# Performance work log

Hardware: AMD Instinct MI355X
Metric: run time of the kernel (lower is better)

The kernel has to match this reference:

```python
import jax, jax.numpy as jnp
import numpy as np

B, L, C = 128, 1000, 12      # batch, seq_len, input_channels
H = 128                       # lstm_hidden
DM, DS, DC = 128, 16, 4       # d_model, d_state, d_conv
DI = 2 * DM                   # d_inner = expand * d_model
DR = 8                        # dt_rank = ceil(d_model/16)
FC, NC = 128, 5               # fc_hidden_size, num_classes


def setup_inputs() -> dict:
    key = jax.random.key(0)
    ks = jax.random.split(key, 24)
    def rn(k, shape, fan):
        return jax.random.normal(k, shape, jnp.float32) / np.sqrt(fan)
    inp = {}
    inp["x"] = jax.random.normal(ks[0], (B, L, C), jnp.float32)
    # LSTM (single layer, batch_first) — PyTorch gate order i,f,g,o
    inp["W_ih"] = rn(ks[1], (4 * H, C), H)
    inp["W_hh"] = rn(ks[2], (4 * H, H), H)
    inp["b_ih"] = rn(ks[3], (4 * H,), H)
    inp["b_hh"] = rn(ks[4], (4 * H,), H)
    # input_proj: Linear(H, DM)
    inp["Wp"] = rn(ks[5], (DM, H), H)
    inp["bp"] = rn(ks[6], (DM,), H)
    # Mamba params
    inp["in_proj_w"] = rn(ks[7], (2 * DI, DM), DM)
    inp["conv_w"] = rn(ks[8], (DI, 1, DC), DC)        # depthwise conv kernel
    inp["conv_b"] = rn(ks[9], (DI,), DC)
    inp["x_proj_w"] = rn(ks[10], (DR + 2 * DS, DI), DI)
    inp["dt_proj_w"] = rn(ks[11], (DI, DR), DR)
    inp["dt_proj_b"] = rn(ks[12], (DI,), DR)
    inp["A_log"] = jnp.broadcast_to(jnp.log(jnp.arange(1, DS + 1, dtype=jnp.float32)), (DI, DS)).copy()
    inp["D"] = jnp.ones((DI,), jnp.float32)
    inp["out_proj_w"] = rn(ks[13], (DM, DI), DI)
    # classifier head
    inp["fc1_w"] = rn(ks[14], (FC, DM), DM)
    inp["fc1_b"] = rn(ks[15], (FC,), DM)
    inp["fc2_w"] = rn(ks[16], (NC, FC), FC)
    inp["fc2_b"] = rn(ks[17], (NC,), FC)
    return inp


def _lstm(x, W_ih, W_hh, b_ih, b_hh):
    b = b_ih + b_hh
    xg = jnp.einsum('blc,gc->blg', x, W_ih) + b  # precompute input gates (B,L,4H)
    def step(carry, xt):
        h, c = carry
        g = xt + h @ W_hh.T
        i, f, gg, o = jnp.split(g, 4, axis=-1)
        c = jax.nn.sigmoid(f) * c + jax.nn.sigmoid(i) * jnp.tanh(gg)
        h = jax.nn.sigmoid(o) * jnp.tanh(c)
        return (h, c), h
    h0 = jnp.zeros((x.shape[0], H), x.dtype)
    (_, _), hs = jax.lax.scan(step, (h0, h0), jnp.swapaxes(xg, 0, 1))
    return jnp.swapaxes(hs, 0, 1)  # (B,L,H)


def _mamba(u, in_proj_w, conv_w, conv_b, x_proj_w, dt_proj_w, dt_proj_b, A_log, D, out_proj_w):
    xz = jnp.einsum('bld,ed->ble', u, in_proj_w)           # (B,L,2*DI)
    xi, z = jnp.split(xz, 2, axis=-1)
    # causal depthwise conv1d over time
    xc = jnp.swapaxes(xi, 1, 2)                             # (B,DI,L)
    xc = jax.lax.conv_general_dilated(xc, conv_w, (1,), [(DC - 1, 0)],
                                      feature_group_count=DI,
                                      dimension_numbers=('NCH', 'OIH', 'NCH'))
    xc = xc + conv_b[None, :, None]
    xs = jax.nn.silu(jnp.swapaxes(xc, 1, 2))                # (B,L,DI)
    x_dbl = jnp.einsum('bld,ed->ble', xs, x_proj_w)         # (B,L,DR+2*DS)
    dt, Bm, Cm = jnp.split(x_dbl, [DR, DR + DS], axis=-1)
    delta = jax.nn.softplus(jnp.einsum('blr,dr->bld', dt, dt_proj_w) + dt_proj_b)  # (B,L,DI)
    A = -jnp.exp(A_log)                                     # (DI,DS)
    def step(h, inp):
        d_t, B_t, C_t, x_t = inp                            # (B,DI),(B,DS),(B,DS),(B,DI)
        dA = jnp.exp(d_t[:, :, None] * A)                   # (B,DI,DS)
        h = dA * h + (d_t * x_t)[:, :, None] * B_t[:, None, :]
        y = jnp.einsum('bds,bs->bd', h, C_t)
        return h, y
    h0 = jnp.zeros((u.shape[0], DI, DS), u.dtype)
    seq = (jnp.swapaxes(delta, 0, 1), jnp.swapaxes(Bm, 0, 1),
           jnp.swapaxes(Cm, 0, 1), jnp.swapaxes(xs, 0, 1))
    _, ys = jax.lax.scan(step, h0, seq)                     # (L,B,DI)
    y = jnp.swapaxes(ys, 0, 1) + xs * D
    y = y * jax.nn.silu(z)
    return jnp.einsum('bld,ed->ble', y, out_proj_w)         # (B,L,DM)


def reference(x, W_ih, W_hh, b_ih, b_hh, Wp, bp, in_proj_w, conv_w, conv_b,
              x_proj_w, dt_proj_w, dt_proj_b, A_log, D, out_proj_w,
              fc1_w, fc1_b, fc2_w, fc2_b):
    h = _lstm(x, W_ih, W_hh, b_ih, b_hh)
    m_in = jnp.einsum('blh,dh->bld', h, Wp) + bp
    m_out = _mamba(m_in, in_proj_w, conv_w, conv_b, x_proj_w,
                   dt_proj_w, dt_proj_b, A_log, D, out_proj_w)
    pooled = m_out.mean(axis=1)                             # (B,DM)
    hfc = jax.nn.relu(pooled @ fc1_w.T + fc1_b)             # dropout: eval mode (identity)
    return hfc @ fc2_w.T + fc2_b                            # (B,NC)
```

## Files before the change

kernel.cpp:

```cpp
#include <hip/hip_runtime.h>
#include <cstdint>
#include <cstddef>

constexpr int LSEQ = 1000;
constexpr int NB   = 128;
constexpr int CINP = 12;
constexpr int HID  = 128;
constexpr int NGATE = 4 * HID;
constexpr int DMOD = 128;
constexpr int DINN = 256;
constexpr int NCL  = 5;

typedef unsigned short ushort_t;
typedef _Float16 half2_t __attribute__((ext_vector_type(2)));

__device__ __forceinline__ float bf2f(ushort_t u) {
  uint32_t b = ((uint32_t)u) << 16;
  float f; __builtin_memcpy(&f, &b, 4); return f;
}
__device__ __forceinline__ ushort_t f2bf(float f) {
  uint32_t b; __builtin_memcpy(&b, &f, 4);
  uint32_t r = (b + 0x7fffu + ((b >> 16) & 1u)) >> 16;
  return (ushort_t)r;
}
__device__ __forceinline__ half2_t u2h2(uint32_t v) {
  half2_t h; __builtin_memcpy(&h, &v, 4); return h;
}
__device__ __forceinline__ uint32_t h22u(half2_t h) {
  uint32_t v; __builtin_memcpy(&v, &h, 4); return v;
}
__device__ __forceinline__ uint32_t bfpair_to_h2(uint32_t v) {
  half2_t h;
  h.x = (_Float16)bf2f((ushort_t)(v & 0xffff));
  h.y = (_Float16)bf2f((ushort_t)(v >> 16));
  return h22u(h);
}

#if __has_builtin(__builtin_amdgcn_fdot2)
__device__ __forceinline__ float FDOT2(half2_t a, half2_t b, float c) {
  return __builtin_amdgcn_fdot2(a, b, c, false);
}
#else
__device__ __forceinline__ float FDOT2(half2_t a, half2_t b, float c) {
  return c + (float)a.x * (float)b.x + (float)a.y * (float)b.y;
}
#endif

__device__ __forceinline__ void bar_lgkm() {
  asm volatile("s_waitcnt lgkmcnt(0)\n\ts_barrier" ::: "memory");
}

__global__ __launch_bounds__(256) void k0_weff(
    const float* __restrict__ ipw, const float* __restrict__ Wp,
    const float* __restrict__ bp, uint32_t* __restrict__ Weffh,
    float* __restrict__ beff) {
  int idx = blockIdx.x * 256 + threadIdx.x;
  if (idx < NGATE * 64) {
    int e = idx >> 6, j = idx & 63;
    float a0 = 0.f, a1 = 0.f;
    for (int d = 0; d < DMOD; ++d) {
      float w = ipw[e * DMOD + d];
      a0 += w * Wp[d * HID + 2 * j];
      a1 += w * Wp[d * HID + 2 * j + 1];
    }
    half2_t h; h.x = (_Float16)a0; h.y = (_Float16)a1;
    Weffh[idx] = h22u(h);
  }
  if (idx < NGATE) {
    float acc = 0.f;
    for (int d = 0; d < DMOD; ++d) acc += ipw[idx * DMOD + d] * bp[d];
    beff[idx] = acc;
  }
}

__global__ __launch_bounds__(256, 1) void k1_lstm(
    const float* __restrict__ x, const float* __restrict__ W_ih,
    const float* __restrict__ W_hh, const float* __restrict__ b_ih,
    const float* __restrict__ b_hh, ushort_t* __restrict__ hout) {
  __shared__ __align__(16) float x_sh[LSEQ * CINP];
  __shared__ __align__(16) ushort_t h_sh[HID];
  __shared__ float tg_sh[HID];
  __shared__ float so_sh[HID];
  const int t = threadIdx.x;
  const int u = t & 127;
  const int half = t >> 7;
  const int rA = u + half * 256;
  const int rB = rA + 128;
  const int b = blockIdx.x;

  const float4* xg4 = reinterpret_cast<const float4*>(x + (size_t)b * LSEQ * CINP);
  float4* xs4 = reinterpret_cast<float4*>(x_sh);
  for (int i = t; i < LSEQ * CINP / 4; i += 256) xs4[i] = xg4[i];

  half2_t wa2[64], wb2[64];
  {
    const float4* wa4 = reinterpret_cast<const float4*>(W_hh) + rA * (HID / 4);
    const float4* wb4 = reinterpret_cast<const float4*>(W_hh) + rB * (HID / 4);
#pragma unroll
    for (int k = 0; k < HID / 4; ++k) {
      float4 v = wa4[k];
      half2_t a; a.x = (_Float16)v.x; a.y = (_Float16)v.y;
      half2_t c; c.x = (_Float16)v.z; c.y = (_Float16)v.w;
      wa2[2 * k] = a; wa2[2 * k + 1] = c;
      float4 w = wb4[k];
      half2_t d; d.x = (_Float16)w.x; d.y = (_Float16)w.y;
      half2_t e; e.x = (_Float16)w.z; e.y = (_Float16)w.w;
      wb2[2 * k] = d; wb2[2 * k + 1] = e;
    }
  }
  float wia[CINP], wib[CINP];
#pragma unroll
  for (int c = 0; c < CINP; ++c) {
    wia[c] = W_ih[rA * CINP + c];
    wib[c] = W_ih[rB * CINP + c];
  }
  const float biasA = b_ih[rA] + b_hh[rA];
  const float biasB = b_ih[rB] + b_hh[rB];

  float cstate = 0.f;
  if (t < HID) h_sh[t] = 0;
  __syncthreads();

  for (int l = 0; l < LSEQ; ++l) {
    const float* xr = &x_sh[l * CINP];
    float pa0 = biasA, pa1 = 0.f, pa2 = 0.f, pa3 = 0.f;
    float pb0 = biasB, pb1 = 0.f, pb2 = 0.f, pb3 = 0.f;
#pragma unroll
    for (int c = 0; c < CINP; c += 4) {
      float x0 = xr[c], x1 = xr[c + 1], x2 = xr[c + 2], x3 = xr[c + 3];
      pa0 += x0 * wia[c];     pa1 += x1 * wia[c + 1];
      pa2 += x2 * wia[c + 2]; pa3 += x3 * wia[c + 3];
      pb0 += x0 * wib[c];     pb1 += x1 * wib[c + 1];
      pb2 += x2 * wib[c + 2]; pb3 += x3 * wib[c + 3];
    }
    const uint4* h4 = reinterpret_cast<const uint4*>(h_sh);
#pragma unroll
    for (int kk = 0; kk < 16; ++kk) {
      uint4 hv = h4[kk];
      half2_t h0 = u2h2(hv.x), h1 = u2h2(hv.y), h2 = u2h2(hv.z), h3 = u2h2(hv.w);
      pa0 = FDOT2(h0, wa2[4 * kk],     pa0);
      pa1 = FDOT2(h1, wa2[4 * kk + 1], pa1);
      pa2 = FDOT2(h2, wa2[4 * kk + 2], pa2);
      pa3 = FDOT2(h3, wa2[4 * kk + 3], pa3);
      pb0 = FDOT2(h0, wb2[4 * kk],     pb0);
      pb1 = FDOT2(h1, wb2[4 * kk + 1], pb1);
      pb2 = FDOT2(h2, wb2[4 * kk + 2], pb2);
      pb3 = FDOT2(h3, wb2[4 * kk + 3], pb3);
    }
    float gA = (pa0 + pa1) + (pa2 + pa3);
    float gB = (pb0 + pb1) + (pb2 + pb3);

    float si = 0.f, sf = 0.f;
    if (half) {
      float tg = 1.f - 2.f / (__expf(2.f * gA) + 1.f);
      float so = 1.f / (1.f + __expf(-gB));
      tg_sh[u] = tg;
      so_sh[u] = so;
    } else {
      si = 1.f / (1.f + __expf(-gA));
      sf = 1.f / (1.f + __expf(-gB));
    }
    bar_lgkm();
    if (!half) {
      cstate = sf * cstate + si * tg_sh[u];
      float th = 1.f - 2.f / (__expf(2.f * cstate) + 1.f);
      float hv = so_sh[u] * th;
      _Float16 hh = (_Float16)hv;
      ushort_t hb; __builtin_memcpy(&hb, &hh, 2);
      h_sh[u] = hb;
      hout[((size_t)b * LSEQ + l) * HID + u] = f2bf(hv);
    }
    bar_lgkm();
  }
}

__global__ __launch_bounds__(256) void k2f(
    const ushort_t* __restrict__ hbuf, const uint32_t* __restrict__ Weffh,
    const float* __restrict__ beff, const float* __restrict__ cw,
    const float* __restrict__ cb, ushort_t* __restrict__ xs,
    ushort_t* __restrict__ sz) {
  constexpr int S = 66;
  __shared__ __align__(16) uint32_t smem[2 * 64 * S];
  uint32_t* As = smem;
  uint32_t* Bs = smem + 64 * S;
  const int tid = threadIdx.x;
  const size_t m0 = (size_t)blockIdx.x * 64;
  const int n0 = blockIdx.y * 64;

  const uint4* h4g = reinterpret_cast<const uint4*>(hbuf);
  for (int i = tid; i < 64 * 16; i += 256) {
    int row = i >> 4, c = i & 15;
    uint4 v = h4g[(m0 + row) * 16 + c];
    uint32_t* p = &As[row * S + c * 4];
    p[0] = bfpair_to_h2(v.x); p[1] = bfpair_to_h2(v.y);
    p[2] = bfpair_to_h2(v.z); p[3] = bfpair_to_h2(v.w);
  }
  const uint4* w4g = reinterpret_cast<const uint4*>(Weffh);
  for (int i = tid; i < 64 * 16; i += 256) {
    int row = i >> 4, c = i & 15;
    uint4 v = w4g[(size_t)(n0 + row) * 16 + c];
    uint32_t* p = &Bs[row * S + c * 4];
    p[0] = v.x; p[1] = v.y; p[2] = v.z; p[3] = v.w;
  }
  __syncthreads();

  const int tx = tid & 15, ty = tid >> 4;
  float acc[4][4] = {};
  {
    const uint32_t* ap = &As[(ty * 4) * S];
    const uint32_t* bp = &Bs[(tx * 4) * S];
#pragma unroll 4
    for (int kk = 0; kk < 32; ++kk) {
      uint2 a0 = *reinterpret_cast<const uint2*>(&ap[kk * 2]);
      uint2 a1 = *reinterpret_cast<const uint2*>(&ap[S + kk * 2]);
      uint2 a2 = *reinterpret_cast<const uint2*>(&ap[2 * S + kk * 2]);
      uint2 a3 = *reinterpret_cast<const uint2*>(&ap[3 * S + kk * 2]);
      uint2 b0 = *reinterpret_cast<const uint2*>(&bp[kk * 2]);
      uint2 b1 = *reinterpret_cast<const uint2*>(&bp[S + kk * 2]);
      uint2 b2 = *reinterpret_cast<const uint2*>(&bp[2 * S + kk * 2]);
      uint2 b3 = *reinterpret_cast<const uint2*>(&bp[3 * S + kk * 2]);
      acc[0][0] = FDOT2(u2h2(a0.x), u2h2(b0.x), acc[0][0]);
      acc[0][1] = FDOT2(u2h2(a0.x), u2h2(b1.x), acc[0][1]);
      acc[0][2] = FDOT2(u2h2(a0.x), u2h2(b2.x), acc[0][2]);
      acc[0][3] = FDOT2(u2h2(a0.x), u2h2(b3.x), acc[0][3]);
      acc[1][0] = FDOT2(u2h2(a1.x), u2h2(b0.x), acc[1][0]);
      acc[1][1] = FDOT2(u2h2(a1.x), u2h2(b1.x), acc[1][1]);
      acc[1][2] = FDOT2(u2h2(a1.x), u2h2(b2.x), acc[1][2]);
      acc[1][3] = FDOT2(u2h2(a1.x), u2h2(b3.x), acc[1][3]);
      acc[2][0] = FDOT2(u2h2(a2.x), u2h2(b0.x), acc[2][0]);
      acc[2][1] = FDOT2(u2h2(a2.x), u2h2(b1.x), acc[2][1]);
      acc[2][2] = FDOT2(u2h2(a2.x), u2h2(b2.x), acc[2][2]);
      acc[2][3] = FDOT2(u2h2(a2.x), u2h2(b3.x), acc[2][3]);
      acc[3][0] = FDOT2(u2h2(a3.x), u2h2(b0.x), acc[3][0]);
      acc[3][1] = FDOT2(u2h2(a3.x), u2h2(b1.x), acc[3][1]);
      acc[3][2] = FDOT2(u2h2(a3.x), u2h2(b2.x), acc[3][2]);
      acc[3][3] = FDOT2(u2h2(a3.x), u2h2(b3.x), acc[3][3]);
      acc[0][0] = FDOT2(u2h2(a0.y), u2h2(b0.y), acc[0][0]);
      acc[0][1] = FDOT2(u2h2(a0.y), u2h2(b1.y), acc[0][1]);
      acc[0][2] = FDOT2(u2h2(a0.y), u2h2(b2.y), acc[0][2]);
      acc[0][3] = FDOT2(u2h2(a0.y), u2h2(b3.y), acc[0][3]);
      acc[1][0] = FDOT2(u2h2(a1.y), u2h2(b0.y), acc[1][0]);
      acc[1][1] = FDOT2(u2h2(a1.y), u2h2(b1.y), acc[1][1]);
      acc[1][2] = FDOT2(u2h2(a1.y), u2h2(b2.y), acc[1][2]);
      acc[1][3] = FDOT2(u2h2(a1.y), u2h2(b3.y), acc[1][3]);
      acc[2][0] = FDOT2(u2h2(a2.y), u2h2(b0.y), acc[2][0]);
      acc[2][1] = FDOT2(u2h2(a2.y), u2h2(b1.y), acc[2][1]);
      acc[2][2] = FDOT2(u2h2(a2.y), u2h2(b2.y), acc[2][2]);
      acc[2][3] = FDOT2(u2h2(a2.y), u2h2(b3.y), acc[2][3]);
      acc[3][0] = FDOT2(u2h2(a3.y), u2h2(b0.y), acc[3][0]);
      acc[3][1] = FDOT2(u2h2(a3.y), u2h2(b1.y), acc[3][1]);
      acc[3][2] = FDOT2(u2h2(a3.y), u2h2(b2.y), acc[3][2]);
      acc[3][3] = FDOT2(u2h2(a3.y), u2h2(b3.y), acc[3][3]);
    }
  }

  const int col = n0 + tx * 4;
  float4 be = *reinterpret_cast<const float4*>(&beff[col]);

  if (n0 >= 256) {
#pragma unroll
    for (int i = 0; i < 4; ++i) {
      size_t row = m0 + ty * 4 + i;
      float v0 = acc[i][0] + be.x, v1 = acc[i][1] + be.y;
      float v2 = acc[i][2] + be.z, v3 = acc[i][3] + be.w;
      ushort4 o;
      o.x = f2bf(v0 / (1.f + __expf(-v0)));
      o.y = f2bf(v1 / (1.f + __expf(-v1)));
      o.z = f2bf(v2 / (1.f + __expf(-v2)));
      o.w = f2bf(v3 / (1.f + __expf(-v3)));
      *reinterpret_cast<ushort4*>(&sz[row * 256 + (col - 256)]) = o;
    }
    return;
  }

  float haloval = 0.f;
  const int hc = tid & 63;
  if (tid < 192) {
    int hr = tid >> 6;
    long hrow = (long)m0 - 3 + hr;
    if (hrow < 0) hrow = 0;
    const uint4* hg = reinterpret_cast<const uint4*>(hbuf + (size_t)hrow * 128);
    const uint32_t* brow = &Bs[hc * S];
    float a0 = beff[n0 + hc], a1 = 0.f, a2 = 0.f, a3 = 0.f;
#pragma unroll
    for (int k = 0; k < 16; ++k) {
      uint4 hv = hg[k];
      a0 = FDOT2(u2h2(bfpair_to_h2(hv.x)), u2h2(brow[4 * k]),     a0);
      a1 = FDOT2(u2h2(bfpair_to_h2(hv.y)), u2h2(brow[4 * k + 1]), a1);
      a2 = FDOT2(u2h2(bfpair_to_h2(hv.z)), u2h2(brow[4 * k + 2]), a2);
      a3 = FDOT2(u2h2(bfpair_to_h2(hv.w)), u2h2(brow[4 * k + 3]), a3);
    }
    haloval = (a0 + a1) + (a2 + a3);
  }
  __syncthreads();

  float* X = reinterpret_cast<float*>(smem);
#pragma unroll
  for (int i = 0; i < 4; ++i) {
    int r = ty * 4 + i;
    float* q = &X[(r + 3) * 68 + tx * 4];
    q[0] = acc[i][0] + be.x; q[1] = acc[i][1] + be.y;
    q[2] = acc[i][2] + be.z; q[3] = acc[i][3] + be.w;
  }
  if (tid < 192) X[(tid >> 6) * 68 + hc] = haloval;
  __syncthreads();

  float cw0[4], cw1[4], cw2[4], cw3[4], cbv[4];
#pragma unroll
  for (int j = 0; j < 4; ++j) {
    int d = col + j;
    cw0[j] = cw[d * 4]; cw1[j] = cw[d * 4 + 1];
    cw2[j] = cw[d * 4 + 2]; cw3[j] = cw[d * 4 + 3];
    cbv[j] = cb[d];
  }
#pragma unroll
  for (int i = 0; i < 4; ++i) {
    int r = ty * 4 + i;
    size_t m = m0 + r;
    int l = (int)(m % LSEQ);
    const float* xr3 = &X[(r + 3) * 68 + tx * 4];
    ushort_t ov[4];
#pragma unroll
    for (int j = 0; j < 4; ++j) {
      float o0 = cbv[j];
      o0 += cw3[j] * xr3[j];
      if (l >= 1) o0 += cw2[j] * xr3[j - 68];
      if (l >= 2) o0 += cw1[j] * xr3[j - 136];
      if (l >= 3) o0 += cw0[j] * xr3[j - 204];
      ov[j] = f2bf(o0 / (1.f + __expf(-o0)));
    }
    ushort4 o; o.x = ov[0]; o.y = ov[1]; o.z = ov[2]; o.w = ov[3];
    *reinterpret_cast<ushort4*>(&xs[m * 256 + col]) = o;
  }
}

__global__ __launch_bounds__(256) void k4_xdbl(
    const ushort_t* __restrict__ xs, const float* __restrict__ xpw,
    float* __restrict__ dtg, float* __restrict__ bc) {
  constexpr int XSTR = 134;
  __shared__ __align__(16) uint32_t xsh[64 * XSTR];
  __shared__ __align__(16) uint32_t wsh[40 * 128];
  const int tid = threadIdx.x;
  const size_t r0 = (size_t)blockIdx.x * 64;

  for (int i = tid; i < 64 * 128; i += 256) {
    int row = i >> 7, kk = i & 127;
    uint32_t v = *reinterpret_cast<const uint32_t*>(&xs[(r0 + row) * 256 + kk * 2]);
    xsh[row * XSTR + kk] = bfpair_to_h2(v);
  }
  for (int i = tid; i < 40 * 128; i += 256) {
    int c = i >> 7, kk = i & 127;
    half2_t h;
    h.x = (_Float16)xpw[c * 256 + kk * 2];
    h.y = (_Float16)xpw[c * 256 + kk * 2 + 1];
    wsh[i] = h22u(h);
  }
  __syncthreads();

  const int row = tid & 63;
  const int cg = tid >> 6;
  float acc[10] = {};
  for (int kk2 = 0; kk2 < 64; ++kk2) {
    uint2 xv = *reinterpret_cast<const uint2*>(&xsh[row * XSTR + kk2 * 2]);
    half2_t x0 = u2h2(xv.x), x1 = u2h2(xv.y);
#pragma unroll
    for (int i = 0; i < 10; ++i) {
      uint2 wv = *reinterpret_cast<const uint2*>(&wsh[(cg + 4 * i) * 128 + kk2 * 2]);
      acc[i] = FDOT2(x0, u2h2(wv.x), acc[i]);
      acc[i] = FDOT2(x1, u2h2(wv.y), acc[i]);
    }
  }
#pragma unroll
  for (int i = 0; i < 10; ++i) {
    int c = cg + 4 * i;
    if (c < 8) dtg[(r0 + row) * 8 + c] = acc[i];
    else bc[(r0 + row) * 32 + (c - 8)] = acc[i];
  }
}

__global__ __launch_bounds__(256) void k5_scan(
    const float* __restrict__ dtg, const ushort_t* __restrict__ xs,
    const ushort_t* __restrict__ sz, const float* __restrict__ bc,
    const float* __restrict__ A_log, const float* __restrict__ Dv,
    const float* __restrict__ dtw, const float* __restrict__ dtb,
    float* __restrict__ ysum) {
  const int b  = blockIdx.x >> 3;
  const int d  = ((blockIdx.x & 7) << 5) + (threadIdx.x >> 3);
  const int sg = threadIdx.x & 7;

  const float Aa0 = -__expf(A_log[d * 16 + sg * 2]);
  const float Aa1 = -__expf(A_log[d * 16 + sg * 2 + 1]);
  float w8[8];
#pragma unroll
  for (int r = 0; r < 8; ++r) w8[r] = dtw[d * 8 + r];
  const float db = dtb[d];
  const float DD = Dv[d];

  float h0 = 0.f, h1 = 0.f;
  float acc = 0.f, accD = 0.f;
  const size_t base = (size_t)b * LSEQ;

  float4 dta_c = *reinterpret_cast<const float4*>(&dtg[base * 8]);
  float4 dtb_c = *reinterpret_cast<const float4*>(&dtg[base * 8 + 4]);
  float  xv_c  = bf2f(xs[base * 256 + d]);
  float  zv_c  = bf2f(sz[base * 256 + d]);
  float2 bv_c  = *reinterpret_cast<const float2*>(&bc[base * 32 + sg * 2]);
  float2 cv_c  = *reinterpret_cast<const float2*>(&bc[base * 32 + 16 + sg * 2]);

  for (int l = 0; l < LSEQ; ++l) {
    const size_t nrow = base + ((l + 1 < LSEQ) ? (l + 1) : l);
    float4 dta_n = *reinterpret_cast<const float4*>(&dtg[nrow * 8]);
    float4 dtb_n = *reinterpret_cast<const float4*>(&dtg[nrow * 8 + 4]);
    float  xv_n  = bf2f(xs[nrow * 256 + d]);
    float  zv_n  = bf2f(sz[nrow * 256 + d]);
    float2 bv_n  = *reinterpret_cast<const float2*>(&bc[nrow * 32 + sg * 2]);
    float2 cv_n  = *reinterpret_cast<const float2*>(&bc[nrow * 32 + 16 + sg * 2]);

    float a = db + dta_c.x * w8[0] + dta_c.y * w8[1] + dta_c.z * w8[2] + dta_c.w * w8[3]
                 + dtb_c.x * w8[4] + dtb_c.y * w8[5] + dtb_c.z * w8[6] + dtb_c.w * w8[7];
    float dl = (a > 20.f) ? a : __logf(1.f + __expf(a));
    float dx = dl * xv_c;
    h0 = __expf(dl * Aa0) * h0 + dx * bv_c.x;
    h1 = __expf(dl * Aa1) * h1 + dx * bv_c.y;
    acc += (h0 * cv_c.x + h1 * cv_c.y) * zv_c;
    accD += xv_c * zv_c;

    dta_c = dta_n; dtb_c = dtb_n;
    xv_c = xv_n; zv_c = zv_n; bv_c = bv_n; cv_c = cv_n;
  }
  if (sg == 0) acc += DD * accD;
  acc += __shfl_xor(acc, 1);
  acc += __shfl_xor(acc, 2);
  acc += __shfl_xor(acc, 4);
  if (sg == 0) ysum[b * 256 + d] = acc;
}

__global__ __launch_bounds__(128) void k6_head(
    const float* __restrict__ ysum, const float* __restrict__ opw,
    const float* __restrict__ fc1w, const float* __restrict__ fc1b,
    const float* __restrict__ fc2w, const float* __restrict__ fc2b,
    float* __restrict__ out) {
  __shared__ float ys[256], pool[128], fcs[128];
  const int b = blockIdx.x, t = threadIdx.x;
  for (int i = t; i < 256; i += 128) ys[i] = ysum[b * 256 + i];
  __syncthreads();
  float a = 0.f;
  for (int e = 0; e < 256; ++e) a += opw[t * 256 + e] * ys[e];
  pool[t] = a * (1.0f / (float)LSEQ);
  __syncthreads();
  float a1 = fc1b[t];
  for (int d2 = 0; d2 < 128; ++d2) a1 += fc1w[t * 128 + d2] * pool[d2];
  fcs[t] = fmaxf(a1, 0.f);
  __syncthreads();
  if (t < NCL) {
    float o = fc2b[t];
    for (int f = 0; f < 128; ++f) o += fc2w[t * 128 + f] * fcs[f];
    out[b * NCL + t] = o;
  }
}

extern "C" void kernel_launch(void* const* d_in, const int* in_sizes, int n_in,
                              void* d_out, int out_size, void* d_ws, size_t ws_size,
                              hipStream_t stream) {
  const float* x     = (const float*)d_in[0];
  const float* W_ih  = (const float*)d_in[1];
  const float* W_hh  = (const float*)d_in[2];
  const float* b_ih  = (const float*)d_in[3];
  const float* b_hh  = (const float*)d_in[4];
  const float* Wp    = (const float*)d_in[5];
  const float* bp    = (const float*)d_in[6];
  const float* ipw   = (const float*)d_in[7];
  const float* cw    = (const float*)d_in[8];
  const float* cb    = (const float*)d_in[9];
  const float* xpw   = (const float*)d_in[10];
  const float* dtw   = (const float*)d_in[11];
  const float* dtb   = (const float*)d_in[12];
  const float* A_log = (const float*)d_in[13];
  const float* Dv    = (const float*)d_in[14];
  const float* opw   = (const float*)d_in[15];
  const float* fc1w  = (const float*)d_in[16];
  const float* fc1b  = (const float*)d_in[17];
  const float* fc2w  = (const float*)d_in[18];
  const float* fc2b  = (const float*)d_in[19];
  float* out = (float*)d_out;

  const size_t A_WEFF = 131072;
  const size_t A_BEFF = 4096, A_YSUM = 131072;
  const size_t A_HBUF = (size_t)NB * LSEQ * HID * 2;
  const size_t A_XS   = (size_t)NB * LSEQ * DINN * 2;
  const size_t A_SZ   = A_XS;
  const size_t A_DT   = (size_t)NB * LSEQ * 8 * 4;
  const size_t A_BC   = (size_t)NB * LSEQ * 32 * 4;
  const size_t FIXED_WIDE = A_WEFF + A_BEFF + A_YSUM + A_HBUF + A_XS + A_SZ + A_DT + A_BC;

  if (FIXED_WIDE <= ws_size) {
    char* p = (char*)d_ws;
    uint32_t* Weffh = (uint32_t*)p; p += A_WEFF;
    float*    beff = (float*)p;    p += A_BEFF;
    float*    ysum = (float*)p;    p += A_YSUM;
    ushort_t* hbuf = (ushort_t*)p; p += A_HBUF;
    ushort_t* xsb  = (ushort_t*)p; p += A_XS;
    ushort_t* szb  = (ushort_t*)p; p += A_SZ;
    float*    dtg  = (float*)p;    p += A_DT;
    float*    bcb  = (float*)p;    p += A_BC;

    const int rows = NB * LSEQ;
    hipLaunchKernelGGL(k0_weff, dim3(128), dim3(256), 0, stream, ipw, Wp, bp, Weffh, beff);
    hipLaunchKernelGGL(k1_lstm, dim3(NB), dim3(256), 0, stream, x, W_ih, W_hh, b_ih, b_hh, hbuf);
    hipLaunchKernelGGL(k2f, dim3(rows / 64, 8), dim3(256), 0, stream,
                       hbuf, Weffh, beff, cw, cb, xsb, szb);
    hipLaunchKernelGGL(k4_xdbl, dim3(rows / 64), dim3(256), 0, stream,
                       xsb, xpw, dtg, bcb);
    hipLaunchKernelGGL(k5_scan, dim3(NB * 8), dim3(256), 0, stream,
                       dtg, xsb, szb, bcb, A_log, Dv, dtw, dtb, ysum);
    hipLaunchKernelGGL(k6_head, dim3(NB), dim3(128), 0, stream,
                       ysum, opw, fc1w, fc1b, fc2w, fc2b, out);
    return;
  }

  const size_t FIXED = A_WEFF + A_BEFF + A_YSUM + A_HBUF;
  const size_t PERB = (size_t)LSEQ * DINN * 2 * 2 + (size_t)LSEQ * 8 * 4 + (size_t)LSEQ * 32 * 4;
  int nb = 8;
  for (int c = 64; c >= 8; c >>= 1) {
    if (FIXED + (size_t)c * PERB <= ws_size) { nb = c; break; }
  }
  char* p = (char*)d_ws;
  uint32_t* Weffh = (uint32_t*)p; p += A_WEFF;
  float*    beff = (float*)p;    p += A_BEFF;
  float*    ysum = (float*)p;    p += A_YSUM;
  ushort_t* hbuf = (ushort_t*)p; p += A_HBUF;
  ushort_t* xsb  = (ushort_t*)p; p += (size_t)nb * LSEQ * DINN * 2;
  ushort_t* szb  = (ushort_t*)p; p += (size_t)nb * LSEQ * DINN * 2;
  float*    dtg  = (float*)p;    p += (size_t)nb * LSEQ * 8 * 4;
  float*    bcb  = (float*)p;

  hipLaunchKernelGGL(k0_weff, dim3(128), dim3(256), 0, stream, ipw, Wp, bp, Weffh, beff);
  hipLaunchKernelGGL(k1_lstm, dim3(NB), dim3(256), 0, stream, x, W_ih, W_hh, b_ih, b_hh, hbuf);
  for (int b0 = 0; b0 < NB; b0 += nb) {
    const int rows = nb * LSEQ;
    hipLaunchKernelGGL(k2f, dim3(rows / 64, 8), dim3(256), 0, stream,
                       hbuf + (size_t)b0 * LSEQ * HID, Weffh, beff, cw, cb, xsb, szb);
    hipLaunchKernelGGL(k4_xdbl, dim3(rows / 64), dim3(256), 0, stream, xsb, xpw, dtg, bcb);
    hipLaunchKernelGGL(k5_scan, dim3(nb * 8), dim3(256), 0, stream,
                       dtg, xsb, szb, bcb, A_log, Dv, dtw, dtb, ysum + (size_t)b0 * DINN);
  }
  hipLaunchKernelGGL(k6_head, dim3(NB), dim3(128), 0, stream,
                     ysum, opw, fc1w, fc1b, fc2w, fc2b, out);
}
```

Before: 1.507 ms.

## Process two batch sequences per LSTM block to reuse register-resident weights

After: 2.005 ms. +33.1%, slower.

```diff
diff --git a/kernel.cpp b/kernel.cpp
--- a/kernel.cpp
+++ b/kernel.cpp
@@ -77,20 +77,26 @@
     const float* __restrict__ x, const float* __restrict__ W_ih,
     const float* __restrict__ W_hh, const float* __restrict__ b_ih,
     const float* __restrict__ b_hh, ushort_t* __restrict__ hout) {
-  __shared__ __align__(16) float x_sh[LSEQ * CINP];
-  __shared__ __align__(16) ushort_t h_sh[HID];
-  __shared__ float tg_sh[HID];
-  __shared__ float so_sh[HID];
+  __shared__ __align__(16) uint32_t x_sh[2][LSEQ * 6];
+  __shared__ __align__(16) ushort_t h_sh[2][HID];
+  __shared__ float tg_sh[2][HID];
+  __shared__ float so_sh[2][HID];
   const int t = threadIdx.x;
   const int u = t & 127;
   const int half = t >> 7;
   const int rA = u + half * 256;
   const int rB = rA + 128;
-  const int b = blockIdx.x;
-
-  const float4* xg4 = reinterpret_cast<const float4*>(x + (size_t)b * LSEQ * CINP);
-  float4* xs4 = reinterpret_cast<float4*>(x_sh);
-  for (int i = t; i < LSEQ * CINP / 4; i += 256) xs4[i] = xg4[i];
+  const int b0 = blockIdx.x * 2;
+
+#pragma unroll
+  for (int q = 0; q < 2; ++q) {
+    const float2* xg2 = reinterpret_cast<const float2*>(x + (size_t)(b0 + q) * LSEQ * CINP);
+    for (int i = t; i < LSEQ * 6; i += 256) {
+      float2 v = xg2[i];
+      half2_t h; h.x = (_Float16)v.x; h.y = (_Float16)v.y;
+      x_sh[q][i] = h22u(h);
+    }
+  }
 
   half2_t wa2[64], wb2[64];
   {
@@ -108,67 +114,97 @@
       wb2[2 * k] = d; wb2[2 * k + 1] = e;
     }
   }
-  float wia[CINP], wib[CINP];
-#pragma unroll
-  for (int c = 0; c < CINP; ++c) {
-    wia[c] = W_ih[rA * CINP + c];
-    wib[c] = W_ih[rB * CINP + c];
+  half2_t wiaP[6], wibP[6];
+#pragma unroll
+  for (int c = 0; c < 6; ++c) {
+    wiaP[c].x = (_Float16)W_ih[rA * CINP + 2 * c];
+    wiaP[c].y = (_Float16)W_ih[rA * CINP + 2 * c + 1];
+    wibP[c].x = (_Float16)W_ih[rB * CINP + 2 * c];
+    wibP[c].y = (_Float16)W_ih[rB * CINP + 2 * c + 1];
   }
   const float biasA = b_ih[rA] + b_hh[rA];
   const float biasB = b_ih[rB] + b_hh[rB];
 
-  float cstate = 0.f;
-  if (t < HID) h_sh[t] = 0;
+  float cs0 = 0.f, cs1 = 0.f;
+  if (t < HID) { h_sh[0][t] = 0; h_sh[1][t] = 0; }
   __syncthreads();
 
   for (int l = 0; l < LSEQ; ++l) {
-    const float* xr = &x_sh[l * CINP];
-    float pa0 = biasA, pa1 = 0.f, pa2 = 0.f, pa3 = 0.f;
-    float pb0 = biasB, pb1 = 0.f, pb2 = 0.f, pb3 = 0.f;
-#pragma unroll
-    for (int c = 0; c < CINP; c += 4) {
-      float x0 = xr[c], x1 = xr[c + 1], x2 = xr[c + 2], x3 = xr[c + 3];
-      pa0 += x0 * wia[c];     pa1 += x1 * wia[c + 1];
-      pa2 += x2 * wia[c + 2]; pa3 += x3 * wia[c + 3];
-      pb0 += x0 * wib[c];     pb1 += x1 * wib[c + 1];
-      pb2 += x2 * wib[c + 2]; pb3 += x3 * wib[c + 3];
-    }
-    const uint4* h4 = reinterpret_cast<const uint4*>(h_sh);
+    float pa[2][4], pb[2][4];
+#pragma unroll
+    for (int q = 0; q < 2; ++q) {
+      pa[q][0] = biasA; pa[q][1] = 0.f; pa[q][2] = 0.f; pa[q][3] = 0.f;
+      pb[q][0] = biasB; pb[q][1] = 0.f; pb[q][2] = 0.f; pb[q][3] = 0.f;
+      const uint32_t* xr = &x_sh[q][l * 6];
+#pragma unroll
+      for (int c = 0; c < 6; c += 2) {
+        half2_t xv0 = u2h2(xr[c]), xv1 = u2h2(xr[c + 1]);
+        pa[q][0] = FDOT2(xv0, wiaP[c],     pa[q][0]);
+        pa[q][1] = FDOT2(xv1, wiaP[c + 1], pa[q][1]);
+        pb[q][0] = FDOT2(xv0, wibP[c],     pb[q][0]);
+        pb[q][1] = FDOT2(xv1, wibP[c + 1], pb[q][1]);
+      }
+    }
+    const uint4* h40 = reinterpret_cast<const uint4*>(h_sh[0]);
+    const uint4* h41 = reinterpret_cast<const uint4*>(h_sh[1]);
 #pragma unroll
     for (int kk = 0; kk < 16; ++kk) {
-      uint4 hv = h4[kk];
-      half2_t h0 = u2h2(hv.x), h1 = u2h2(hv.y), h2 = u2h2(hv.z), h3 = u2h2(hv.w);
-      pa0 = FDOT2(h0, wa2[4 * kk],     pa0);
-      pa1 = FDOT2(h1, wa2[4 * kk + 1], pa1);
-      pa2 = FDOT2(h2, wa2[4 * kk + 2], pa2);
-      pa3 = FDOT2(h3, wa2[4 * kk + 3], pa3);
-      pb0 = FDOT2(h0, wb2[4 * kk],     pb0);
-      pb1 = FDOT2(h1, wb2[4 * kk + 1], pb1);
-      pb2 = FDOT2(h2, wb2[4 * kk + 2], pb2);
-      pb3 = FDOT2(h3, wb2[4 * kk + 3], pb3);
-    }
-    float gA = (pa0 + pa1) + (pa2 + pa3);
-    float gB = (pb0 + pb1) + (pb2 + pb3);
-
-    float si = 0.f, sf = 0.f;
+      uint4 hv0 = h40[kk];
+      uint4 hv1 = h41[kk];
+      half2_t a0 = u2h2(hv0.x), a1 = u2h2(hv0.y), a2 = u2h2(hv0.z), a3 = u2h2(hv0.w);
+      half2_t c0 = u2h2(hv1.x), c1 = u2h2(hv1.y), c2 = u2h2(hv1.z), c3 = u2h2(hv1.w);
+      pa[0][0] = FDOT2(a0, wa2[4 * kk],     pa[0][0]);
+      pa[1][0] = FDOT2(c0, wa2[4 * kk],     pa[1][0]);
+      pa[0][1] = FDOT2(a1, wa2[4 * kk + 1], pa[0][1]);
+      pa[1][1] = FDOT2(c1, wa2[4 * kk + 1], pa[1][1]);
+      pa[0][2] = FDOT2(a2, wa2[4 * kk + 2], pa[0][2]);
+      pa[1][2] = FDOT2(c2, wa2[4 * kk + 2], pa[1][2]);
+      pa[0][3] = FDOT2(a3, wa2[4 * kk + 3], pa[0][3]);
+      pa[1][3] = FDOT2(c3, wa2[4 * kk + 3], pa[1][3]);
+      pb[0][0] = FDOT2(a0, wb2[4 * kk],     pb[0][0]);
+      pb[1][0] = FDOT2(c0, wb2[4 * kk],     pb[1][0]);
+      pb[0][1] = FDOT2(a1, wb2[4 * kk + 1], pb[0][1]);
+      pb[1][1] = FDOT2(c1, wb2[4 * kk + 1], pb[1][1]);
+      pb[0][2] = FDOT2(a2, wb2[4 * kk + 2], pb[0][2]);
+      pb[1][2] = FDOT2(c2, wb2[4 * kk + 2], pb[1][2]);
+      pb[0][3] = FDOT2(a3, wb2[4 * kk + 3], pb[0][3]);
+      pb[1][3] = FDOT2(c3, wb2[4 * kk + 3], pb[1][3]);
+    }
+    float gA0 = (pa[0][0] + pa[0][1]) + (pa[0][2] + pa[0][3]);
+    float gB0 = (pb[0][0] + pb[0][1]) + (pb[0][2] + pb[0][3]);
+    float gA1 = (pa[1][0] + pa[1][1]) + (pa[1][2] + pa[1][3]);
+    float gB1 = (pb[1][0] + pb[1][1]) + (pb[1][2] + pb[1][3]);
+
+    float si0 = 0.f, sf0 = 0.f, si1 = 0.f, sf1 = 0.f;
     if (half) {
-      float tg = 1.f - 2.f / (__expf(2.f * gA) + 1.f);
-      float so = 1.f / (1.f + __expf(-gB));
-      tg_sh[u] = tg;
-      so_sh[u] = so;
+      float tg0 = 1.f - 2.f / (__expf(2.f * gA0) + 1.f);
+      float tg1 = 1.f - 2.f / (__expf(2.f * gA1) + 1.f);
+      float so0 = 1.f / (1.f + __expf(-gB0));
+      float so1 = 1.f / (1.f + __expf(-gB1));
+      tg_sh[0][u] = tg0; tg_sh[1][u] = tg1;
+      so_sh[0][u] = so0; so_sh[1][u] = so1;
     } else {
-      si = 1.f / (1.f + __expf(-gA));
-      sf = 1.f / (1.f + __expf(-gB));
+      si0 = 1.f / (1.f + __expf(-gA0));
+      si1 = 1.f / (1.f + __expf(-gA1));
+      sf0 = 1.f / (1.f + __expf(-gB0));
+      sf1 = 1.f / (1.f + __expf(-gB1));
     }
     bar_lgkm();
     if (!half) {
-      cstate = sf * cstate + si * tg_sh[u];
-      float th = 1.f - 2.f / (__expf(2.f * cstate) + 1.f);
-      float hv = so_sh[u] * th;
-      _Float16 hh = (_Float16)hv;
-      ushort_t hb; __builtin_memcpy(&hb, &hh, 2);
-      h_sh[u] = hb;
-      hout[((size_t)b * LSEQ + l) * HID + u] = f2bf(hv);
+      cs0 = sf0 * cs0 + si0 * tg_sh[0][u];
+      cs1 = sf1 * cs1 + si1 * tg_sh[1][u];
+      float th0 = 1.f - 2.f / (__expf(2.f * cs0) + 1.f);
+      float th1 = 1.f - 2.f / (__expf(2.f * cs1) + 1.f);
+      float hv0 = so_sh[0][u] * th0;
+      float hv1 = so_sh[1][u] * th1;
+      _Float16 hh0 = (_Float16)hv0, hh1 = (_Float16)hv1;
+      ushort_t hb0, hb1;
+      __builtin_memcpy(&hb0, &hh0, 2);
+      __builtin_memcpy(&hb1, &hh1, 2);
+      h_sh[0][u] = hb0;
+      h_sh[1][u] = hb1;
+      hout[((size_t)b0 * LSEQ + l) * HID + u] = f2bf(hv0);
+      hout[((size_t)(b0 + 1) * LSEQ + l) * HID + u] = f2bf(hv1);
     }
     bar_lgkm();
   }
@@ -506,7 +542,7 @@
 
     const int rows = NB * LSEQ;
     hipLaunchKernelGGL(k0_weff, dim3(128), dim3(256), 0, stream, ipw, Wp, bp, Weffh, beff);
-    hipLaunchKernelGGL(k1_lstm, dim3(NB), dim3(256), 0, stream, x, W_ih, W_hh, b_ih, b_hh, hbuf);
+    hipLaunchKernelGGL(k1_lstm, dim3(NB / 2), dim3(256), 0, stream, x, W_ih, W_hh, b_ih, b_hh, hbuf);
     hipLaunchKernelGGL(k2f, dim3(rows / 64, 8), dim3(256), 0, stream,
                        hbuf, Weffh, beff, cw, cb, xsb, szb);
     hipLaunchKernelGGL(k4_xdbl, dim3(rows / 64), dim3(256), 0, stream,
@@ -535,7 +571,7 @@
   float*    bcb  = (float*)p;
 
   hipLaunchKernelGGL(k0_weff, dim3(128), dim3(256), 0, stream, ipw, Wp, bp, Weffh, beff);
-  hipLaunchKernelGGL(k1_lstm, dim3(NB), dim3(256), 0, stream, x, W_ih, W_hh, b_ih, b_hh, hbuf);
+  hipLaunchKernelGGL(k1_lstm, dim3(NB / 2), dim3(256), 0, stream, x, W_ih, W_hh, b_ih, b_hh, hbuf);
   for (int b0 = 0; b0 < NB; b0 += nb) {
     const int rows = nb * LSEQ;
     hipLaunchKernelGGL(k2f, dim3(rows / 64, 8), dim3(256), 0, stream,
```
